# Kernel tuning notes

Hardware: AMD Instinct MI355X
Metric: run time of the kernel (lower is better)

## Reference

```python
import jax, jax.numpy as jnp
import numpy as np

N = 100000
E = 1200000
NFEAT = 64
NCLASS = 64


def setup_inputs() -> dict:
    key = jax.random.key(0)
    k1, k2, k3, k4, k5, k6 = jax.random.split(key, 6)
    x = jax.random.normal(k1, (N, NFEAT), dtype=jnp.float32)
    edge_row = jax.random.randint(k2, (E,), 0, N, dtype=jnp.int32).astype(jnp.int64)
    edge_col = jax.random.randint(k3, (E,), 0, N, dtype=jnp.int32).astype(jnp.int64)
    edge_weight = jax.random.uniform(k4, (E,), dtype=jnp.float32)
    W = jax.random.normal(k5, (NCLASS, NFEAT), dtype=jnp.float32) / np.sqrt(NFEAT)
    b = jax.random.normal(k6, (NCLASS,), dtype=jnp.float32) * 0.01
    return {"x": x, "edge_row": edge_row, "edge_col": edge_col,
            "edge_weight": edge_weight, "W": W, "b": b, "k": 2}


def _spmm(edge_row, edge_col, edge_weight, x):
    # out[i] = sum_{e: row[e]==i} w[e] * x[col[e]]  == (sparse adj) @ x
    msgs = edge_weight[:, None] * x[edge_col]          # [E, F]
    return jax.ops.segment_sum(msgs, edge_row, num_segments=N)


def reference(x, edge_row, edge_col, edge_weight, W, b, k):
    h = x
    for _ in range(k):  # k is a small static int (propagation depth)
        h = _spmm(edge_row, edge_col, edge_weight, h)
    return h @ W.T + b  # nn.Linear(nfeat, nclass)
```

## Files before the change

kernel.cpp:

```cpp
#include <hip/hip_runtime.h>
#include <hip/hip_fp16.h>

#define FF 64
#define RPB 128
#define RCAP 2048
#define PAIRCAP 2560
#define PCHUNK 8192
#define NBCNT 782

typedef _Float16 f16x8 __attribute__((ext_vector_type(8)));
typedef float    f32x4 __attribute__((ext_vector_type(4)));


union HU { unsigned int u; __half2 h; };

__device__ __forceinline__ unsigned int f2h2(float a, float b) {
    HU t; t.h = __floats2half2_rn(a, b);
    return t.u;
}
__device__ __forceinline__ __half2 u2h2(unsigned int u) {
    HU t; t.u = u;
    return t.h;
}


__global__ void cvt_and_partition(const float* __restrict__ x, unsigned short* __restrict__ xh,
                                  int nelem,
                                  const int* __restrict__ erow, const int* __restrict__ ecol,
                                  const float* __restrict__ ew, int* __restrict__ bcursor,
                                  uint2* __restrict__ bent, int E, int partBlocks) {
    __shared__ int lcnt[NBCNT];
    __shared__ int lbase[NBCNT];
    __shared__ int srow[PCHUNK];
    int t = threadIdx.x;

    if ((int)blockIdx.x >= partBlocks) {
        int i = ((blockIdx.x - partBlocks) * 256 + t) * 4;
        if (i < nelem) {
            float4 v = *(const float4*)&x[i];
            uint2 st;
            st.x = f2h2(v.x, v.y);
            st.y = f2h2(v.z, v.w);
            *(uint2*)&xh[i] = st;
        }
        return;
    }

    for (int i = t; i < NBCNT; i += 256) lcnt[i] = 0;
    __syncthreads();

    int base = blockIdx.x * PCHUNK;
    int lim  = min(PCHUNK, E - base);

    for (int i = t; i < lim; i += 256) {
        int r = erow[base + i];
        srow[i] = r;
        atomicAdd(&lcnt[r >> 7], 1);
    }
    __syncthreads();
    for (int i = t; i < NBCNT; i += 256) {
        int c = lcnt[i];
        lbase[i] = c ? atomicAdd(&bcursor[i], c) : 0;
        lcnt[i] = 0;
    }
    __syncthreads();
    for (int i = t; i < lim; i += 256) {
        int e = base + i;
        int r = srow[i];
        int bkt = r >> 7;
        int off = atomicAdd(&lcnt[bkt], 1);
        uint2 en;
        en.x = ((unsigned)(r & (RPB - 1)) << 17) | (unsigned)ecol[e];
        en.y = (unsigned)__float_as_int(ew[e]);
        bent[(size_t)bkt * RCAP + lbase[bkt] + off] = en;
    }
}


__device__ __forceinline__ void build_lds_csr(const uint2* __restrict__ bent_b, int cnt,
                                              uint2* ent, int2* pairLds,
                                              int* deg, int* pofs, int* cur, int* part,
                                              int t) {
    for (int i = t; i < cnt; i += 256) ent[i] = bent_b[i];
    if (t < RPB) { deg[t] = 0; cur[t] = 0; }
    __syncthreads();
    for (int i = t; i < cnt; i += 256)
        atomicAdd(&deg[ent[i].x >> 17], 1);
    __syncthreads();

    if (t < RPB) part[t] = (deg[t] + 3) & ~3;
    __syncthreads();
    for (int off = 1; off < RPB; off <<= 1) {
        int add = (t < RPB && t >= off) ? part[t - off] : 0;
        __syncthreads();
        if (t < RPB) part[t] += add;
        __syncthreads();
    }
    if (t < RPB) pofs[t] = part[t] - ((deg[t] + 3) & ~3);
    __syncthreads();

    for (int i = t; i < cnt; i += 256) {
        uint2 e = ent[i];
        int lr  = e.x >> 17;
        int col = e.x & 0x1FFFF;
        float w = __int_as_float((int)e.y);
        int pos = pofs[lr] + atomicAdd(&cur[lr], 1);
        pairLds[pos] = make_int2(col, (int)f2h2(w, w));
    }
    if (t < RPB) {
        int a = deg[t], p = (a + 3) & ~3;
        for (int q = a; q < p; ++q) pairLds[pofs[t] + q] = make_int2(0, 0);
    }
    __syncthreads();
}


__device__ __forceinline__ void pkfma4(__half2 w2, uint4 v, __half2 acc[4]) {
    acc[0] = __hfma2(w2, u2h2(v.x), acc[0]);
    acc[1] = __hfma2(w2, u2h2(v.y), acc[1]);
    acc[2] = __hfma2(w2, u2h2(v.z), acc[2]);
    acc[3] = __hfma2(w2, u2h2(v.w), acc[3]);
}

__device__ __forceinline__ void row_accum8_lds(const int4* __restrict__ p, int n4,
                                               const uint4* __restrict__ hin4,
                                               int lg, __half2 acc[4]) {
    if (n4 <= 0) return;
    int4 q0 = p[0];
    int4 q1 = p[1];
    uint4 v0 = hin4[(size_t)q0.x * 8 + lg];
    uint4 v1 = hin4[(size_t)q0.z * 8 + lg];
    uint4 v2 = hin4[(size_t)q1.x * 8 + lg];
    uint4 v3 = hin4[(size_t)q1.z * 8 + lg];
    for (int i = 2; i < n4; i += 2) {
        int4 r0 = p[i];
        int4 r1 = p[i + 1];
        uint4 u0 = hin4[(size_t)r0.x * 8 + lg];
        uint4 u1 = hin4[(size_t)r0.z * 8 + lg];
        uint4 u2 = hin4[(size_t)r1.x * 8 + lg];
        uint4 u3 = hin4[(size_t)r1.z * 8 + lg];
        pkfma4(u2h2((unsigned)q0.y), v0, acc);
        pkfma4(u2h2((unsigned)q0.w), v1, acc);
        pkfma4(u2h2((unsigned)q1.y), v2, acc);
        pkfma4(u2h2((unsigned)q1.w), v3, acc);
        q0 = r0; q1 = r1;
        v0 = u0; v1 = u1; v2 = u2; v3 = u3;
    }
    pkfma4(u2h2((unsigned)q0.y), v0, acc);
    pkfma4(u2h2((unsigned)q0.w), v1, acc);
    pkfma4(u2h2((unsigned)q1.y), v2, acc);
    pkfma4(u2h2((unsigned)q1.w), v3, acc);
}


__global__ __launch_bounds__(256) void spmm1(const uint2* __restrict__ bent,
        const int* __restrict__ bcount, const unsigned short* __restrict__ hin,
        unsigned short* __restrict__ hout, int Nn) {
    __shared__ uint2 ent[RCAP];
    __shared__ int2  pairLds[PAIRCAP];
    __shared__ int   deg[RPB], pofs[RPB], cur[RPB], part[RPB];
    const uint4* hin4 = (const uint4*)hin;
    int b = blockIdx.x, t = threadIdx.x;
    int cnt = min(bcount[b], RCAP);

    build_lds_csr(bent + (size_t)b * RCAP, cnt, ent, pairLds, deg, pofs, cur, part, t);

    int lane = t & 63, g = lane >> 3, lg = lane & 7;
    int rbase = (t >> 6) * 8 + g;
#pragma unroll
    for (int pass = 0; pass < 4; ++pass) {
        int rloc = pass * 32 + rbase;
        int row  = b * RPB + rloc;
        __half2 acc[4] = {__half2{0,0}, __half2{0,0}, __half2{0,0}, __half2{0,0}};
        int plen = (deg[rloc] + 3) & ~3;
        row_accum8_lds((const int4*)pairLds + (pofs[rloc] >> 1), plen >> 1, hin4, lg, acc);
        if (row < Nn)
            ((uint4*)hout)[(size_t)row * 8 + lg] = *(const uint4*)acc;
    }
}


__global__ __launch_bounds__(256) void spmm2(const uint2* __restrict__ bent,
        const int* __restrict__ bcount, const unsigned short* __restrict__ hin,
        const float* __restrict__ Wm, const float* __restrict__ bias,
        float* __restrict__ out, int Nn) {
    __shared__ __align__(16) char ublob[27904];
    __shared__ int2 pairLds[PAIRCAP];
    __shared__ int  deg[RPB], pofs[RPB], cur[RPB], part[RPB];
    const uint4* hin4 = (const uint4*)hin;
    int b = blockIdx.x, t = threadIdx.x;
    int cnt = min(bcount[b], RCAP);

    build_lds_csr(bent + (size_t)b * RCAP, cnt, (uint2*)ublob, pairLds,
                  deg, pofs, cur, part, t);

    unsigned short (*shw)[72] = (unsigned short(*)[72])ublob;
    unsigned short (*shh)[72] = (unsigned short(*)[72])(ublob + 9216);
    float* sbias = (float*)(ublob + 9216 + 18432);

    for (int i = t; i < 1024; i += 256) {
        int idx = i * 4;
        int c = idx >> 6, f = idx & 63;
        float4 w4 = *(const float4*)&Wm[idx];
        uint2 pk;
        pk.x = f2h2(w4.x, w4.y);
        pk.y = f2h2(w4.z, w4.w);
        *(uint2*)&shw[c][f] = pk;
    }
    if (t < 64) sbias[t] = bias[t];

    int lane = t & 63, g = lane >> 3, lg = lane & 7;
    int rbase = (t >> 6) * 8 + g;
#pragma unroll
    for (int pass = 0; pass < 4; ++pass) {
        int rloc = pass * 32 + rbase;
        __half2 acc[4] = {__half2{0,0}, __half2{0,0}, __half2{0,0}, __half2{0,0}};
        int plen = (deg[rloc] + 3) & ~3;
        row_accum8_lds((const int4*)pairLds + (pofs[rloc] >> 1), plen >> 1, hin4, lg, acc);
        *(uint4*)&shh[rloc][lg * 8] = *(const uint4*)acc;
    }
    __syncthreads();

    int wid = t >> 6;
    int mr = lane & 15, kg = lane >> 4;
#pragma unroll
    for (int ti = 0; ti < 2; ++ti) {
        int tt = wid + ti * 4;
        f32x4 c0 = {0.f,0.f,0.f,0.f}, c1 = {0.f,0.f,0.f,0.f};
        f32x4 c2 = {0.f,0.f,0.f,0.f}, c3 = {0.f,0.f,0.f,0.f};
#pragma unroll
        for (int kc = 0; kc < 2; ++kc) {
            int k0 = kc * 32 + kg * 8;
            f16x8 a  = *(const f16x8*)&shh[tt * 16 + mr][k0];
            f16x8 b0 = *(const f16x8*)&shw[mr][k0];
            f16x8 b1 = *(const f16x8*)&shw[16 + mr][k0];
            f16x8 b2 = *(const f16x8*)&shw[32 + mr][k0];
            f16x8 b3 = *(const f16x8*)&shw[48 + mr][k0];
            c0 = __builtin_amdgcn_mfma_f32_16x16x32_f16(a, b0, c0, 0, 0, 0);
            c1 = __builtin_amdgcn_mfma_f32_16x16x32_f16(a, b1, c1, 0, 0, 0);
            c2 = __builtin_amdgcn_mfma_f32_16x16x32_f16(a, b2, c2, 0, 0, 0);
            c3 = __builtin_amdgcn_mfma_f32_16x16x32_f16(a, b3, c3, 0, 0, 0);
        }
#pragma unroll
        for (int j = 0; j < 4; ++j) {
            int orow = b * RPB + tt * 16 + kg * 4 + j;
            if (orow < Nn) {
                float* op = &out[(size_t)orow * FF];
                op[mr]      = c0[j] + sbias[mr];
                op[16 + mr] = c1[j] + sbias[16 + mr];
                op[32 + mr] = c2[j] + sbias[32 + mr];
                op[48 + mr] = c3[j] + sbias[48 + mr];
            }
        }
    }
}


extern "C" void kernel_launch(void* const* d_in, const int* in_sizes, int n_in,
                              void* d_out, int out_size, void* d_ws, size_t ws_size,
                              hipStream_t stream) {
    const float* x    = (const float*)d_in[0];
    const int*   erow = (const int*)  d_in[1];
    const int*   ecol = (const int*)  d_in[2];
    const float* ew   = (const float*)d_in[3];
    const float* W    = (const float*)d_in[4];
    const float* b    = (const float*)d_in[5];

    int E  = in_sizes[1];
    int Nn = in_sizes[0] / FF;
    int nelem = Nn * FF;
    int NB = (Nn + RPB - 1) / RPB;

    char*  ws  = (char*)d_ws;
    size_t off = 0;
    auto alloc = [&](size_t bytes) { void* p = ws + off; off += (bytes + 255) & ~255ULL; return p; };
    unsigned short* xh   = (unsigned short*)alloc((size_t)nelem * 2);
    unsigned short* h1h  = (unsigned short*)alloc((size_t)nelem * 2);
    uint2*          bent = (uint2*)alloc((size_t)NB * RCAP * sizeof(uint2));
    int*            bcursor = (int*)alloc(NBCNT * sizeof(int));

    hipMemsetAsync(bcursor, 0, NBCNT * sizeof(int), stream);

    int partBlocks = (E + PCHUNK - 1) / PCHUNK;
    int cvtBlocks  = (nelem / 4 + 255) / 256;
    cvt_and_partition<<<partBlocks + cvtBlocks, 256, 0, stream>>>(
        x, xh, nelem, erow, ecol, ew, bcursor, bent, E, partBlocks);

    spmm1<<<NB, 256, 0, stream>>>(bent, bcursor, xh, h1h, Nn);
    spmm2<<<NB, 256, 0, stream>>>(bent, bcursor, h1h, W, b, (float*)d_out, Nn);
}
```

Measured before the change: 102.9 us.

## Use 512-thread SpMM blocks, build CSR directly from global, split cvt kernel

SpMM blocks grow from 256 to 512 threads, so each wave handles two row passes instead of four and each wave does one MFMA tile. The LDS staging copy of bucket entries is dropped: the CSR build reads entries straight from global memory, cutting shared memory per block and LDS traffic. The fused convert+partition kernel is split into two separate launches, which adds a launch and removes overlap between the two jobs. PAIRCAP is reduced, which risks overflow when a bucket's padded degree total is large.

```diff
diff --git a/kernel.cpp b/kernel.cpp
--- a/kernel.cpp
+++ b/kernel.cpp
@@ -4,7 +4,7 @@
 #define FF 64
 #define RPB 128
 #define RCAP 2048
-#define PAIRCAP 2560
+#define PAIRCAP 2432
 #define PCHUNK 8192
 #define NBCNT 782
 
@@ -24,27 +24,25 @@
 }
 
 
-__global__ void cvt_and_partition(const float* __restrict__ x, unsigned short* __restrict__ xh,
-                                  int nelem,
-                                  const int* __restrict__ erow, const int* __restrict__ ecol,
-                                  const float* __restrict__ ew, int* __restrict__ bcursor,
-                                  uint2* __restrict__ bent, int E, int partBlocks) {
+__global__ void cvt_f16(const float* __restrict__ x, unsigned short* __restrict__ xh, int n) {
+    int i = (blockIdx.x * blockDim.x + threadIdx.x) * 4;
+    if (i < n) {
+        float4 v = *(const float4*)&x[i];
+        uint2 st;
+        st.x = f2h2(v.x, v.y);
+        st.y = f2h2(v.z, v.w);
+        *(uint2*)&xh[i] = st;
+    }
+}
+
+
+__global__ void bucket_partition(const int* __restrict__ erow, const int* __restrict__ ecol,
+                                 const float* __restrict__ ew, int* __restrict__ bcursor,
+                                 uint2* __restrict__ bent, int E) {
     __shared__ int lcnt[NBCNT];
     __shared__ int lbase[NBCNT];
     __shared__ int srow[PCHUNK];
     int t = threadIdx.x;
-
-    if ((int)blockIdx.x >= partBlocks) {
-        int i = ((blockIdx.x - partBlocks) * 256 + t) * 4;
-        if (i < nelem) {
-            float4 v = *(const float4*)&x[i];
-            uint2 st;
-            st.x = f2h2(v.x, v.y);
-            st.y = f2h2(v.z, v.w);
-            *(uint2*)&xh[i] = st;
-        }
-        return;
-    }
 
     for (int i = t; i < NBCNT; i += 256) lcnt[i] = 0;
     __syncthreads();
@@ -77,15 +75,13 @@
 }
 
 
-__device__ __forceinline__ void build_lds_csr(const uint2* __restrict__ bent_b, int cnt,
-                                              uint2* ent, int2* pairLds,
-                                              int* deg, int* pofs, int* cur, int* part,
-                                              int t) {
-    for (int i = t; i < cnt; i += 256) ent[i] = bent_b[i];
+__device__ __forceinline__ void build_lds_csr_g(const uint2* __restrict__ src, int cnt,
+                                                int2* pairLds, int* deg, int* pofs,
+                                                int* cur, int* part, int t, int nthr) {
     if (t < RPB) { deg[t] = 0; cur[t] = 0; }
     __syncthreads();
-    for (int i = t; i < cnt; i += 256)
-        atomicAdd(&deg[ent[i].x >> 17], 1);
+    for (int i = t; i < cnt; i += nthr)
+        atomicAdd(&deg[src[i].x >> 17], 1);
     __syncthreads();
 
     if (t < RPB) part[t] = (deg[t] + 3) & ~3;
@@ -99,8 +95,8 @@
     if (t < RPB) pofs[t] = part[t] - ((deg[t] + 3) & ~3);
     __syncthreads();
 
-    for (int i = t; i < cnt; i += 256) {
-        uint2 e = ent[i];
+    for (int i = t; i < cnt; i += nthr) {
+        uint2 e = src[i];
         int lr  = e.x >> 17;
         int col = e.x & 0x1FFFF;
         float w = __int_as_float((int)e.y);
@@ -153,23 +149,22 @@
 }
 
 
-__global__ __launch_bounds__(256) void spmm1(const uint2* __restrict__ bent,
+__global__ __launch_bounds__(512) void spmm1(const uint2* __restrict__ bent,
         const int* __restrict__ bcount, const unsigned short* __restrict__ hin,
         unsigned short* __restrict__ hout, int Nn) {
-    __shared__ uint2 ent[RCAP];
-    __shared__ int2  pairLds[PAIRCAP];
-    __shared__ int   deg[RPB], pofs[RPB], cur[RPB], part[RPB];
+    __shared__ int2 pairLds[PAIRCAP];
+    __shared__ int  deg[RPB], pofs[RPB], cur[RPB], part[RPB];
     const uint4* hin4 = (const uint4*)hin;
     int b = blockIdx.x, t = threadIdx.x;
     int cnt = min(bcount[b], RCAP);
 
-    build_lds_csr(bent + (size_t)b * RCAP, cnt, ent, pairLds, deg, pofs, cur, part, t);
+    build_lds_csr_g(bent + (size_t)b * RCAP, cnt, pairLds, deg, pofs, cur, part, t, 512);
 
     int lane = t & 63, g = lane >> 3, lg = lane & 7;
     int rbase = (t >> 6) * 8 + g;
 #pragma unroll
-    for (int pass = 0; pass < 4; ++pass) {
-        int rloc = pass * 32 + rbase;
+    for (int pass = 0; pass < 2; ++pass) {
+        int rloc = pass * 64 + rbase;
         int row  = b * RPB + rloc;
         __half2 acc[4] = {__half2{0,0}, __half2{0,0}, __half2{0,0}, __half2{0,0}};
         int plen = (deg[rloc] + 3) & ~3;
@@ -180,25 +175,20 @@
 }
 
 
-__global__ __launch_bounds__(256) void spmm2(const uint2* __restrict__ bent,
+__global__ __launch_bounds__(512) void spmm2(const uint2* __restrict__ bent,
         const int* __restrict__ bcount, const unsigned short* __restrict__ hin,
         const float* __restrict__ Wm, const float* __restrict__ bias,
         float* __restrict__ out, int Nn) {
-    __shared__ __align__(16) char ublob[27904];
     __shared__ int2 pairLds[PAIRCAP];
     __shared__ int  deg[RPB], pofs[RPB], cur[RPB], part[RPB];
+    __shared__ unsigned short shw[64][72];
+    __shared__ unsigned short shh[128][72];
+    __shared__ float sbias[64];
     const uint4* hin4 = (const uint4*)hin;
     int b = blockIdx.x, t = threadIdx.x;
     int cnt = min(bcount[b], RCAP);
 
-    build_lds_csr(bent + (size_t)b * RCAP, cnt, (uint2*)ublob, pairLds,
-                  deg, pofs, cur, part, t);
-
-    unsigned short (*shw)[72] = (unsigned short(*)[72])ublob;
-    unsigned short (*shh)[72] = (unsigned short(*)[72])(ublob + 9216);
-    float* sbias = (float*)(ublob + 9216 + 18432);
-
-    for (int i = t; i < 1024; i += 256) {
+    for (int i = t; i < 1024; i += 512) {
         int idx = i * 4;
         int c = idx >> 6, f = idx & 63;
         float4 w4 = *(const float4*)&Wm[idx];
@@ -209,11 +199,13 @@
     }
     if (t < 64) sbias[t] = bias[t];
 
+    build_lds_csr_g(bent + (size_t)b * RCAP, cnt, pairLds, deg, pofs, cur, part, t, 512);
+
     int lane = t & 63, g = lane >> 3, lg = lane & 7;
     int rbase = (t >> 6) * 8 + g;
 #pragma unroll
-    for (int pass = 0; pass < 4; ++pass) {
-        int rloc = pass * 32 + rbase;
+    for (int pass = 0; pass < 2; ++pass) {
+        int rloc = pass * 64 + rbase;
         __half2 acc[4] = {__half2{0,0}, __half2{0,0}, __half2{0,0}, __half2{0,0}};
         int plen = (deg[rloc] + 3) & ~3;
         row_accum8_lds((const int4*)pairLds + (pofs[rloc] >> 1), plen >> 1, hin4, lg, acc);
@@ -221,36 +213,32 @@
     }
     __syncthreads();
 
-    int wid = t >> 6;
+    int tt = t >> 6;
     int mr = lane & 15, kg = lane >> 4;
-#pragma unroll
-    for (int ti = 0; ti < 2; ++ti) {
-        int tt = wid + ti * 4;
-        f32x4 c0 = {0.f,0.f,0.f,0.f}, c1 = {0.f,0.f,0.f,0.f};
-        f32x4 c2 = {0.f,0.f,0.f,0.f}, c3 = {0.f,0.f,0.f,0.f};
-#pragma unroll
-        for (int kc = 0; kc < 2; ++kc) {
-            int k0 = kc * 32 + kg * 8;
-            f16x8 a  = *(const f16x8*)&shh[tt * 16 + mr][k0];
-            f16x8 b0 = *(const f16x8*)&shw[mr][k0];
-            f16x8 b1 = *(const f16x8*)&shw[16 + mr][k0];
-            f16x8 b2 = *(const f16x8*)&shw[32 + mr][k0];
-            f16x8 b3 = *(const f16x8*)&shw[48 + mr][k0];
-            c0 = __builtin_amdgcn_mfma_f32_16x16x32_f16(a, b0, c0, 0, 0, 0);
-            c1 = __builtin_amdgcn_mfma_f32_16x16x32_f16(a, b1, c1, 0, 0, 0);
-            c2 = __builtin_amdgcn_mfma_f32_16x16x32_f16(a, b2, c2, 0, 0, 0);
-            c3 = __builtin_amdgcn_mfma_f32_16x16x32_f16(a, b3, c3, 0, 0, 0);
-        }
-#pragma unroll
-        for (int j = 0; j < 4; ++j) {
-            int orow = b * RPB + tt * 16 + kg * 4 + j;
-            if (orow < Nn) {
-                float* op = &out[(size_t)orow * FF];
-                op[mr]      = c0[j] + sbias[mr];
-                op[16 + mr] = c1[j] + sbias[16 + mr];
-                op[32 + mr] = c2[j] + sbias[32 + mr];
-                op[48 + mr] = c3[j] + sbias[48 + mr];
-            }
+    f32x4 c0 = {0.f,0.f,0.f,0.f}, c1 = {0.f,0.f,0.f,0.f};
+    f32x4 c2 = {0.f,0.f,0.f,0.f}, c3 = {0.f,0.f,0.f,0.f};
+#pragma unroll
+    for (int kc = 0; kc < 2; ++kc) {
+        int k0 = kc * 32 + kg * 8;
+        f16x8 a  = *(const f16x8*)&shh[tt * 16 + mr][k0];
+        f16x8 b0 = *(const f16x8*)&shw[mr][k0];
+        f16x8 b1 = *(const f16x8*)&shw[16 + mr][k0];
+        f16x8 b2 = *(const f16x8*)&shw[32 + mr][k0];
+        f16x8 b3 = *(const f16x8*)&shw[48 + mr][k0];
+        c0 = __builtin_amdgcn_mfma_f32_16x16x32_f16(a, b0, c0, 0, 0, 0);
+        c1 = __builtin_amdgcn_mfma_f32_16x16x32_f16(a, b1, c1, 0, 0, 0);
+        c2 = __builtin_amdgcn_mfma_f32_16x16x32_f16(a, b2, c2, 0, 0, 0);
+        c3 = __builtin_amdgcn_mfma_f32_16x16x32_f16(a, b3, c3, 0, 0, 0);
+    }
+#pragma unroll
+    for (int j = 0; j < 4; ++j) {
+        int orow = b * RPB + tt * 16 + kg * 4 + j;
+        if (orow < Nn) {
+            float* op = &out[(size_t)orow * FF];
+            op[mr]      = c0[j] + sbias[mr];
+            op[16 + mr] = c1[j] + sbias[16 + mr];
+            op[32 + mr] = c2[j] + sbias[32 + mr];
+            op[48 + mr] = c3[j] + sbias[48 + mr];
         }
     }
 }
@@ -281,11 +269,10 @@
 
     hipMemsetAsync(bcursor, 0, NBCNT * sizeof(int), stream);
 
-    int partBlocks = (E + PCHUNK - 1) / PCHUNK;
-    int cvtBlocks  = (nelem / 4 + 255) / 256;
-    cvt_and_partition<<<partBlocks + cvtBlocks, 256, 0, stream>>>(
-        x, xh, nelem, erow, ecol, ew, bcursor, bent, E, partBlocks);
-
-    spmm1<<<NB, 256, 0, stream>>>(bent, bcursor, xh, h1h, Nn);
-    spmm2<<<NB, 256, 0, stream>>>(bent, bcursor, h1h, W, b, (float*)d_out, Nn);
-}
+    cvt_f16<<<(nelem / 4 + 255) / 256, 256, 0, stream>>>(x, xh, nelem);
+    bucket_partition<<<(E + PCHUNK - 1) / PCHUNK, 256, 0, stream>>>(erow, ecol, ew,
+                                                                    bcursor, bent, E);
+
+    spmm1<<<NB, 512, 0, stream>>>(bent, bcursor, xh, h1h, Nn);
+    spmm2<<<NB, 512, 0, stream>>>(bent, bcursor, h1h, W, b, (float*)d_out, Nn);
+}
```

Result: no change. 103.8 us (+0.9%).
